# Optimization experiments

Hardware: AMD Instinct MI355X
Metric: run time of the kernel (lower is better)

## Reference

```python
import jax, jax.numpy as jnp
import numpy as np

N_NODES = 50000
N_EDGES = 800000
NUM_REL = 3
NUM_GRAPHS = 512


def _rgcn(x, src, dst, edge_type, Wrel, Wroot, b):
    # PyG RGCNConv with default aggr='mean':
    # out[i] = x[i] @ Wroot + b + sum_r mean_{j in N_r(i)} x[j] @ Wrel[r]
    out = x @ Wroot + b
    for r in range(NUM_REL):
        mask = (edge_type == r)
        h = x @ Wrel[r]                      # transform nodes first (N x d), cheaper than per-edge
        msg = jnp.where(mask[:, None], h[src], jnp.zeros((), x.dtype))  # [E, hid]
        sums = jax.ops.segment_sum(msg, dst, num_segments=N_NODES)
        cnt = jax.ops.segment_sum(mask.astype(x.dtype), dst, num_segments=N_NODES)
        out = out + sums / jnp.maximum(cnt, 1.0)[:, None]
    return out


def setup_inputs() -> dict:
    key = jax.random.key(0)
    ks = jax.random.split(key, 12)
    d, hid, classes = 96, 96, 16
    x = jax.random.normal(ks[0], (N_NODES, d), dtype=jnp.float32)
    edge_index = jax.random.randint(ks[1], (2, N_EDGES), 0, N_NODES, dtype=jnp.int64)
    edge_type = jax.random.randint(ks[2], (N_EDGES,), 0, NUM_REL, dtype=jnp.int64)
    batch = jnp.sort(jax.random.randint(ks[3], (N_NODES,), 0, NUM_GRAPHS, dtype=jnp.int64))
    s1 = 1.0 / np.sqrt(d)
    s2 = 1.0 / np.sqrt(hid)
    return {
        "x": x,
        "edge_index": edge_index,
        "edge_type": edge_type,
        "batch": batch,
        "Wrel1": jax.random.normal(ks[4], (NUM_REL, d, hid), dtype=jnp.float32) * s1,
        "Wroot1": jax.random.normal(ks[5], (d, hid), dtype=jnp.float32) * s1,
        "b1": jnp.zeros((hid,), dtype=jnp.float32),
        "Wrel2": jax.random.normal(ks[6], (NUM_REL, hid, hid), dtype=jnp.float32) * s2,
        "Wroot2": jax.random.normal(ks[7], (hid, hid), dtype=jnp.float32) * s2,
        "b2": jnp.zeros((hid,), dtype=jnp.float32),
        "Wlin": jax.random.normal(ks[8], (hid, classes), dtype=jnp.float32) * s2,
        "blin": jnp.zeros((classes,), dtype=jnp.float32),
    }


def reference(x, edge_index, edge_type, batch, Wrel1, Wroot1, b1, Wrel2, Wroot2, b2, Wlin, blin):
    src, dst = edge_index[0], edge_index[1]
    h = jax.nn.relu(_rgcn(x, src, dst, edge_type, Wrel1, Wroot1, b1))
    h = jax.nn.relu(_rgcn(h, src, dst, edge_type, Wrel2, Wroot2, b2))
    # global mean pool over graphs
    sums = jax.ops.segment_sum(h, batch, num_segments=NUM_GRAPHS)          # [G, hid]
    cnt = jax.ops.segment_sum(jnp.ones((h.shape[0],), h.dtype), batch, num_segments=NUM_GRAPHS)
    pooled = sums / jnp.maximum(cnt, 1.0)[:, None]
    return pooled @ Wlin + blin
```

## Files before the change

kernel.cpp:

```cpp
#include <hip/hip_runtime.h>


#define THREADS 256

typedef __attribute__((ext_vector_type(8))) short short8v;
typedef __attribute__((ext_vector_type(4))) float f32x4;

__device__ __forceinline__ unsigned short f2bf(float f) {
  union { float f; unsigned u; } v; v.f = f;
  unsigned r = v.u + 0x7FFF + ((v.u >> 16) & 1);
  return (unsigned short)(r >> 16);
}
__device__ __forceinline__ float bf2f(unsigned short b) {
  union { unsigned u; float f; } v; v.u = ((unsigned)b) << 16;
  return v.f;
}
__device__ __forceinline__ float bits2f(unsigned u) {
  union { unsigned u; float f; } v; v.u = u;
  return v.f;
}

__global__ __launch_bounds__(256) void k_packW(
    const float* __restrict__ Wrel1, const float* __restrict__ Wroot1,
    const float* __restrict__ Wrel2, const float* __restrict__ Wroot2,
    unsigned short* __restrict__ PBh, unsigned short* __restrict__ PBl)
{
  int lay = blockIdx.x / 144;
  int idx = (blockIdx.x % 144) * 256 + threadIdx.x;
  const float* Wroot = lay ? Wroot2 : Wroot1;
  const float* Wrel  = lay ? Wrel2  : Wrel1;
  int j    = idx & 7;
  int lane = (idx >> 3) & 63;
  int CT   = (idx >> 9) % 24;
  int ks   = (idx >> 9) / 24;
  int k    = ks * 32 + (lane >> 4) * 8 + j;
  int col  = CT * 16 + (lane & 15);
  int m    = col / 96, jj = col % 96;
  float f  = (m == 0) ? Wroot[k * 96 + jj]
                      : Wrel[((size_t)(m - 1) * 96 + k) * 96 + jj];
  unsigned short h = f2bf(f);
  PBh[(size_t)lay * 36864 + idx] = h;
  PBl[(size_t)lay * 36864 + idx] = f2bf(f - bf2f(h));
}

__global__ __launch_bounds__(256) void k_convX(
    const float4* __restrict__ X4, unsigned short* __restrict__ Xh,
    unsigned short* __restrict__ Xl, int n4)
{
  int i = blockIdx.x * THREADS + threadIdx.x;
  if (i >= n4) return;
  float4 v = X4[i];
  ushort4 h, l;
  h.x = f2bf(v.x); l.x = f2bf(v.x - bf2f(h.x));
  h.y = f2bf(v.y); l.y = f2bf(v.y - bf2f(h.y));
  h.z = f2bf(v.z); l.z = f2bf(v.z - bf2f(h.z));
  h.w = f2bf(v.w); l.w = f2bf(v.w - bf2f(h.w));
  *(ushort4*)(Xh + (size_t)i * 4) = h;
  *(ushort4*)(Xl + (size_t)i * 4) = l;
}

__global__ __launch_bounds__(256) void k_hist(
    const int* __restrict__ ei, const int* __restrict__ et,
    int* __restrict__ cnt, int* __restrict__ rank, int* __restrict__ bucket,
    int E, int N)
{
  int e = blockIdx.x * THREADS + threadIdx.x;
  if (e >= E) return;
  int b = et[e] * N + ei[E + e];
  bucket[e] = b;
  rank[e] = atomicAdd(&cnt[b], 1);
}

__global__ __launch_bounds__(256) void k_scan1(int* __restrict__ data, int* __restrict__ blockSums)
{
  __shared__ int sh[256];
  int tid = threadIdx.x;
  size_t base = (size_t)blockIdx.x * 1024 + (size_t)tid * 4;
  int4 v = *(const int4*)(data + base);
  int i0 = v.x, i1 = i0 + v.y, i2 = i1 + v.z, i3 = i2 + v.w;
  int tsum = i3;
  sh[tid] = tsum;
  __syncthreads();
  for (int off = 1; off < 256; off <<= 1) {
    int t = (tid >= off) ? sh[tid - off] : 0;
    __syncthreads();
    sh[tid] += t;
    __syncthreads();
  }
  int excl = sh[tid] - tsum;
  int4 o; o.x = i0 + excl; o.y = i1 + excl; o.z = i2 + excl; o.w = i3 + excl;
  *(int4*)(data + base) = o;
  if (tid == 255) blockSums[blockIdx.x] = sh[255];
}

__global__ __launch_bounds__(256) void k_scan2(const int* __restrict__ blockSums,
                                               int* __restrict__ blockOffs, int nb)
{
  __shared__ int sh[256];
  int tid = threadIdx.x;
  int v = (tid < nb) ? blockSums[tid] : 0;
  sh[tid] = v;
  __syncthreads();
  for (int off = 1; off < 256; off <<= 1) {
    int t = (tid >= off) ? sh[tid - off] : 0;
    __syncthreads();
    sh[tid] += t;
    __syncthreads();
  }
  blockOffs[tid] = sh[tid] - v;
}

__global__ __launch_bounds__(256) void k_scan3(int* __restrict__ data, const int* __restrict__ blockOffs)
{
  int tid = threadIdx.x;
  size_t base = (size_t)blockIdx.x * 1024 + (size_t)tid * 4;
  int add = blockOffs[blockIdx.x];
  int4 v = *(const int4*)(data + base);
  v.x += add; v.y += add; v.z += add; v.w += add;
  *(int4*)(data + base) = v;
}

__global__ __launch_bounds__(256) void k_scatter(
    const int* __restrict__ ei, const int* __restrict__ offs,
    const int* __restrict__ rank, const int* __restrict__ bucket,
    int* __restrict__ payload, int E)
{
  int e = blockIdx.x * THREADS + threadIdx.x;
  if (e >= E) return;
  int b = bucket[e];
  int base = (b == 0) ? 0 : offs[b - 1];
  payload[base + rank[e]] = ei[e];
}

__global__ __launch_bounds__(256) void k_gemm(
    const unsigned short* __restrict__ Xh, const unsigned short* __restrict__ Xl,
    const unsigned short* __restrict__ PBh, const unsigned short* __restrict__ PBl,
    float* __restrict__ Yroot, unsigned short* __restrict__ Hrel, int nRows)
{
  int wv = threadIdx.x >> 6, lane = threadIdx.x & 63;
  int lr = lane & 15, lq = lane >> 4;
  int r0 = blockIdx.x * 64;

  f32x4 acc[4][6];
#pragma unroll
  for (int rt = 0; rt < 4; ++rt)
#pragma unroll
    for (int ct = 0; ct < 6; ++ct) acc[rt][ct] = (f32x4){0.f, 0.f, 0.f, 0.f};

#pragma unroll 1
  for (int ks = 0; ks < 3; ++ks) {
    short8v Ah[4], Al[4];
#pragma unroll
    for (int rt = 0; rt < 4; ++rt) {
      int row = r0 + rt * 16 + lr;
      if (row >= nRows) row = nRows - 1;
      size_t off = (size_t)row * 96 + ks * 32 + lq * 8;
      Ah[rt] = *(const short8v*)(Xh + off);
      Al[rt] = *(const short8v*)(Xl + off);
    }
#pragma unroll
    for (int ct = 0; ct < 6; ++ct) {
      int CT = wv * 6 + ct;
      size_t boff = ((size_t)(ks * 24 + CT) * 64 + lane) * 8;
      short8v Bh = *(const short8v*)(PBh + boff);
      short8v Bl = *(const short8v*)(PBl + boff);
#pragma unroll
      for (int rt = 0; rt < 4; ++rt) {
        acc[rt][ct] = __builtin_amdgcn_mfma_f32_16x16x32_bf16(Ah[rt], Bh, acc[rt][ct], 0, 0, 0);
        acc[rt][ct] = __builtin_amdgcn_mfma_f32_16x16x32_bf16(Al[rt], Bh, acc[rt][ct], 0, 0, 0);
        acc[rt][ct] = __builtin_amdgcn_mfma_f32_16x16x32_bf16(Ah[rt], Bl, acc[rt][ct], 0, 0, 0);
      }
    }
  }

  if (wv == 0) {
#pragma unroll
    for (int rt = 0; rt < 4; ++rt)
#pragma unroll
      for (int q = 0; q < 4; ++q) {
        int row = r0 + rt * 16 + lq * 4 + q;
        if (row < nRows) {
          float* yp = Yroot + (size_t)row * 96 + lr;
#pragma unroll
          for (int ct = 0; ct < 6; ++ct) yp[ct * 16] = acc[rt][ct][q];
        }
      }
  } else {
    int r = wv - 1;
#pragma unroll
    for (int rt = 0; rt < 4; ++rt)
#pragma unroll
      for (int q = 0; q < 4; ++q) {
        int row = r0 + rt * 16 + lq * 4 + q;
        if (row < nRows) {
          unsigned short* hp = Hrel + ((size_t)r * nRows + row) * 96 + lr;
#pragma unroll
          for (int ct = 0; ct < 6; ++ct) hp[ct * 16] = f2bf(acc[rt][ct][q]);
        }
      }
  }
}

__global__ __launch_bounds__(256) void k_agg3(
    const float* __restrict__ Yroot, const unsigned short* __restrict__ Hrel,
    const int* __restrict__ offs, const int* __restrict__ payload,
    const float* __restrict__ bias,
    unsigned int* outH, unsigned int* outL, unsigned int* outF, int N)
{
  int node = blockIdx.x * 16 + (threadIdx.x >> 4);
  int l = threadIdx.x & 15;
  if (node >= N) return;

  const float2* yp = (const float2*)(Yroot + (size_t)node * 96) + 3 * l;
  const float2* bp = (const float2*)bias + 3 * l;
  float2 y0 = yp[0], y1 = yp[1], y2 = yp[2];
  float2 b0 = bp[0], b1 = bp[1], b2 = bp[2];
  float v[6];
  v[0] = y0.x + b0.x; v[1] = y0.y + b0.y;
  v[2] = y1.x + b1.x; v[3] = y1.y + b1.y;
  v[4] = y2.x + b2.x; v[5] = y2.y + b2.y;

#pragma unroll
  for (int r = 0; r < 3; ++r) {
    int bkt = r * N + node;
    int s = (bkt == 0) ? 0 : offs[bkt - 1];
    int e = offs[bkt];
    const unsigned int* base = (const unsigned int*)(Hrel + (size_t)r * N * 96);
    float a[6] = {0.f, 0.f, 0.f, 0.f, 0.f, 0.f};
    int t = s;
    for (; t + 3 < e; t += 4) {
      int p0 = payload[t], p1 = payload[t + 1], p2 = payload[t + 2], p3 = payload[t + 3];
      const unsigned int* h0 = base + (size_t)p0 * 48 + 3 * l;
      const unsigned int* h1 = base + (size_t)p1 * 48 + 3 * l;
      const unsigned int* h2 = base + (size_t)p2 * 48 + 3 * l;
      const unsigned int* h3 = base + (size_t)p3 * 48 + 3 * l;
      unsigned u0 = h0[0], u1 = h0[1], u2 = h0[2];
      unsigned w0 = h1[0], w1 = h1[1], w2 = h1[2];
      unsigned x0 = h2[0], x1 = h2[1], x2 = h2[2];
      unsigned z0 = h3[0], z1 = h3[1], z2 = h3[2];
      a[0] += bits2f(u0 << 16); a[1] += bits2f(u0 & 0xFFFF0000u);
      a[2] += bits2f(u1 << 16); a[3] += bits2f(u1 & 0xFFFF0000u);
      a[4] += bits2f(u2 << 16); a[5] += bits2f(u2 & 0xFFFF0000u);
      a[0] += bits2f(w0 << 16); a[1] += bits2f(w0 & 0xFFFF0000u);
      a[2] += bits2f(w1 << 16); a[3] += bits2f(w1 & 0xFFFF0000u);
      a[4] += bits2f(w2 << 16); a[5] += bits2f(w2 & 0xFFFF0000u);
      a[0] += bits2f(x0 << 16); a[1] += bits2f(x0 & 0xFFFF0000u);
      a[2] += bits2f(x1 << 16); a[3] += bits2f(x1 & 0xFFFF0000u);
      a[4] += bits2f(x2 << 16); a[5] += bits2f(x2 & 0xFFFF0000u);
      a[0] += bits2f(z0 << 16); a[1] += bits2f(z0 & 0xFFFF0000u);
      a[2] += bits2f(z1 << 16); a[3] += bits2f(z1 & 0xFFFF0000u);
      a[4] += bits2f(z2 << 16); a[5] += bits2f(z2 & 0xFFFF0000u);
    }
    for (; t < e; ++t) {
      const unsigned int* h0 = base + (size_t)payload[t] * 48 + 3 * l;
      unsigned u0 = h0[0], u1 = h0[1], u2 = h0[2];
      a[0] += bits2f(u0 << 16); a[1] += bits2f(u0 & 0xFFFF0000u);
      a[2] += bits2f(u1 << 16); a[3] += bits2f(u1 & 0xFFFF0000u);
      a[4] += bits2f(u2 << 16); a[5] += bits2f(u2 & 0xFFFF0000u);
    }
    float inv = (e > s) ? 1.0f / (float)(e - s) : 0.0f;
#pragma unroll
    for (int i = 0; i < 6; ++i) v[i] += a[i] * inv;
  }
#pragma unroll
  for (int i = 0; i < 6; ++i) v[i] = fmaxf(v[i], 0.f);

  size_t ob = (size_t)node * 48 + 3 * l;
  if (outF) {
    outF[ob]     = ((unsigned)f2bf(v[1]) << 16) | f2bf(v[0]);
    outF[ob + 1] = ((unsigned)f2bf(v[3]) << 16) | f2bf(v[2]);
    outF[ob + 2] = ((unsigned)f2bf(v[5]) << 16) | f2bf(v[4]);
  } else {
    unsigned short h[6], lo[6];
#pragma unroll
    for (int i = 0; i < 6; ++i) { h[i] = f2bf(v[i]); lo[i] = f2bf(v[i] - bf2f(h[i])); }
    outH[ob]     = ((unsigned)h[1] << 16) | h[0];
    outH[ob + 1] = ((unsigned)h[3] << 16) | h[2];
    outH[ob + 2] = ((unsigned)h[5] << 16) | h[4];
    outL[ob]     = ((unsigned)lo[1] << 16) | lo[0];
    outL[ob + 1] = ((unsigned)lo[3] << 16) | lo[2];
    outL[ob + 2] = ((unsigned)lo[5] << 16) | lo[4];
  }
}

__global__ __launch_bounds__(256) void k_poolfinal(
    const unsigned int* __restrict__ H, const int* __restrict__ batch,
    const float* __restrict__ Wlin, const float* __restrict__ blin,
    float* __restrict__ out, int N, int G)
{
  int g = blockIdx.x;
  int tid = threadIdx.x;
  int lo = 0, hi = N;
  while (lo < hi) { int m = (lo + hi) >> 1; if (batch[m] < g) lo = m + 1; else hi = m; }
  int s = lo; hi = N;
  while (lo < hi) { int m = (lo + hi) >> 1; if (batch[m] < g + 1) lo = m + 1; else hi = m; }
  int e = lo;

  int grp = tid >> 4, l = tid & 15;
  float a[6] = {0.f, 0.f, 0.f, 0.f, 0.f, 0.f};
  for (int i = s + grp; i < e; i += 16) {
    const unsigned int* hp = H + (size_t)i * 48 + 3 * l;
    unsigned u0 = hp[0], u1 = hp[1], u2 = hp[2];
    a[0] += bits2f(u0 << 16); a[1] += bits2f(u0 & 0xFFFF0000u);
    a[2] += bits2f(u1 << 16); a[3] += bits2f(u1 & 0xFFFF0000u);
    a[4] += bits2f(u2 << 16); a[5] += bits2f(u2 & 0xFFFF0000u);
  }
  __shared__ float sh[16][96];
  __shared__ float pooled[96];
#pragma unroll
  for (int i = 0; i < 6; ++i) sh[grp][6 * l + i] = a[i];
  __syncthreads();
  if (tid < 96) {
    float t = 0.f;
#pragma unroll
    for (int j = 0; j < 16; ++j) t += sh[j][tid];
    float inv = (e > s) ? 1.0f / (float)(e - s) : 0.0f;
    pooled[tid] = t * inv;
  }
  __syncthreads();
  if (tid < 16) {
    float acc = blin[tid];
    for (int k = 0; k < 96; ++k) acc = fmaf(pooled[k], Wlin[k * 16 + tid], acc);
    out[(size_t)g * 16 + tid] = acc;
  }
}

extern "C" void kernel_launch(void* const* d_in, const int* in_sizes, int n_in,
                              void* d_out, int out_size, void* d_ws, size_t ws_size,
                              hipStream_t stream)
{
  const float* x      = (const float*)d_in[0];
  const int*   ei     = (const int*)d_in[1];
  const int*   et     = (const int*)d_in[2];
  const int*   batch  = (const int*)d_in[3];
  const float* Wrel1  = (const float*)d_in[4];
  const float* Wroot1 = (const float*)d_in[5];
  const float* b1     = (const float*)d_in[6];
  const float* Wrel2  = (const float*)d_in[7];
  const float* Wroot2 = (const float*)d_in[8];
  const float* b2     = (const float*)d_in[9];
  const float* Wlin   = (const float*)d_in[10];
  const float* blin   = (const float*)d_in[11];
  float* out = (float*)d_out;
  (void)n_in; (void)ws_size;

  int N = in_sizes[0] / 96;
  int E = in_sizes[1] / 2;
  int G = out_size / 16;
  int NB = 3 * N;
  int nb1 = (NB + 1023) / 1024;
  int SCAN = nb1 * 1024;

  char* w = (char*)d_ws;
  size_t o = 0;
  auto carve = [&](size_t bytes) -> char* {
    char* p = w + o;
    o = (o + bytes + 255) & ~(size_t)255;
    return p;
  };
  float*          Yroot = (float*)carve((size_t)N * 96 * 4);
  unsigned short* Hrel  = (unsigned short*)carve((size_t)3 * N * 96 * 2);
  unsigned short* Xh    = (unsigned short*)carve((size_t)N * 96 * 2);
  unsigned short* Xl    = (unsigned short*)carve((size_t)N * 96 * 2);
  unsigned short* Hout  = (unsigned short*)carve((size_t)N * 96 * 2);
  unsigned short* PBh   = (unsigned short*)carve((size_t)2 * 36864 * 2);
  unsigned short* PBl   = (unsigned short*)carve((size_t)2 * 36864 * 2);
  int*            offs  = (int*)carve((size_t)SCAN * 4);
  int*            blockSums = (int*)carve(256 * 4);
  int*            blockOffs = (int*)carve(256 * 4);
  int*            rank  = (int*)carve((size_t)E * 4);
  int*            bucket= (int*)carve((size_t)E * 4);
  int*            payload = (int*)carve((size_t)E * 4);

  hipMemsetAsync(offs, 0, (size_t)SCAN * 4, stream);

  k_packW<<<288, THREADS, 0, stream>>>(Wrel1, Wroot1, Wrel2, Wroot2, PBh, PBl);
  k_convX<<<(N * 24 + THREADS - 1) / THREADS, THREADS, 0, stream>>>(
      (const float4*)x, Xh, Xl, N * 24);

  k_hist<<<(E + THREADS - 1) / THREADS, THREADS, 0, stream>>>(ei, et, offs, rank, bucket, E, N);
  k_scan1<<<nb1, THREADS, 0, stream>>>(offs, blockSums);
  k_scan2<<<1, THREADS, 0, stream>>>(blockSums, blockOffs, nb1);
  k_scan3<<<nb1, THREADS, 0, stream>>>(offs, blockOffs);
  k_scatter<<<(E + THREADS - 1) / THREADS, THREADS, 0, stream>>>(ei, offs, rank, bucket, payload, E);

  int gg = (N + 63) / 64;
  int ag = (N + 15) / 16;

  k_gemm<<<gg, THREADS, 0, stream>>>(Xh, Xl, PBh, PBl, Yroot, Hrel, N);
  k_agg3<<<ag, THREADS, 0, stream>>>(Yroot, Hrel, offs, payload, b1,
                                     (unsigned int*)Xh, (unsigned int*)Xl, nullptr, N);
  k_gemm<<<gg, THREADS, 0, stream>>>(Xh, Xl, PBh + 36864, PBl + 36864, Yroot, Hrel, N);
  k_agg3<<<ag, THREADS, 0, stream>>>(Yroot, Hrel, offs, payload, b2,
                                     nullptr, nullptr, (unsigned int*)Hout, N);

  k_poolfinal<<<G, THREADS, 0, stream>>>((const unsigned int*)Hout, batch, Wlin, blin, out, N, G);
}
```

Measured before the change: 303.1 us.

## Fuse prep kernels, convert x inside GEMM, shrink payload, vectorize GEMM stores

Merges weight packing and the edge histogram into a single launch, and drops the separate x-to-bf16 split kernel by converting fp32 x to hi/lo bf16 inside the first GEMM. The neighbour index payload is stored as 16-bit values, halving its gather traffic; this relies on node ids fitting in 16 bits, which does not hold for 50000 nodes beyond 65535? (50000 < 65536, so it fits). GEMM epilogue stores are made contiguous per lane by permuting the column layout, with compensating permutations of layer-2 weights, bias indexing and the final Wlin. Together these aim to cut launch overhead and memory traffic, at the cost of permuted intermediate layouts that must stay consistent.

```diff
diff --git a/kernel.cpp b/kernel.cpp
--- a/kernel.cpp
+++ b/kernel.cpp
@@ -19,56 +19,44 @@
   union { unsigned u; float f; } v; v.u = u;
   return v.f;
 }
-
-__global__ __launch_bounds__(256) void k_packW(
+__device__ __forceinline__ unsigned packbf(float a, float b) {
+  return ((unsigned)f2bf(b) << 16) | f2bf(a);
+}
+
+__global__ __launch_bounds__(256) void k_prep(
     const float* __restrict__ Wrel1, const float* __restrict__ Wroot1,
     const float* __restrict__ Wrel2, const float* __restrict__ Wroot2,
-    unsigned short* __restrict__ PBh, unsigned short* __restrict__ PBl)
-{
-  int lay = blockIdx.x / 144;
-  int idx = (blockIdx.x % 144) * 256 + threadIdx.x;
-  const float* Wroot = lay ? Wroot2 : Wroot1;
-  const float* Wrel  = lay ? Wrel2  : Wrel1;
-  int j    = idx & 7;
-  int lane = (idx >> 3) & 63;
-  int CT   = (idx >> 9) % 24;
-  int ks   = (idx >> 9) / 24;
-  int k    = ks * 32 + (lane >> 4) * 8 + j;
-  int col  = CT * 16 + (lane & 15);
-  int m    = col / 96, jj = col % 96;
-  float f  = (m == 0) ? Wroot[k * 96 + jj]
-                      : Wrel[((size_t)(m - 1) * 96 + k) * 96 + jj];
-  unsigned short h = f2bf(f);
-  PBh[(size_t)lay * 36864 + idx] = h;
-  PBl[(size_t)lay * 36864 + idx] = f2bf(f - bf2f(h));
-}
-
-__global__ __launch_bounds__(256) void k_convX(
-    const float4* __restrict__ X4, unsigned short* __restrict__ Xh,
-    unsigned short* __restrict__ Xl, int n4)
-{
-  int i = blockIdx.x * THREADS + threadIdx.x;
-  if (i >= n4) return;
-  float4 v = X4[i];
-  ushort4 h, l;
-  h.x = f2bf(v.x); l.x = f2bf(v.x - bf2f(h.x));
-  h.y = f2bf(v.y); l.y = f2bf(v.y - bf2f(h.y));
-  h.z = f2bf(v.z); l.z = f2bf(v.z - bf2f(h.z));
-  h.w = f2bf(v.w); l.w = f2bf(v.w - bf2f(h.w));
-  *(ushort4*)(Xh + (size_t)i * 4) = h;
-  *(ushort4*)(Xl + (size_t)i * 4) = l;
-}
-
-__global__ __launch_bounds__(256) void k_hist(
+    unsigned short* __restrict__ PBh, unsigned short* __restrict__ PBl,
     const int* __restrict__ ei, const int* __restrict__ et,
     int* __restrict__ cnt, int* __restrict__ rank, int* __restrict__ bucket,
     int E, int N)
 {
-  int e = blockIdx.x * THREADS + threadIdx.x;
-  if (e >= E) return;
-  int b = et[e] * N + ei[E + e];
-  bucket[e] = b;
-  rank[e] = atomicAdd(&cnt[b], 1);
+  int bid = blockIdx.x;
+  if (bid < 288) {
+    int lay = bid / 144;
+    int idx = (bid % 144) * 256 + threadIdx.x;
+    const float* Wroot = lay ? Wroot2 : Wroot1;
+    const float* Wrel  = lay ? Wrel2  : Wrel1;
+    int j    = idx & 7;
+    int lane = (idx >> 3) & 63;
+    int CT   = (idx >> 9) % 24;
+    int ks   = (idx >> 9) / 24;
+    int kpos = ks * 32 + (lane >> 4) * 8 + j;
+    int k    = lay ? ((kpos % 6) * 16 + kpos / 6) : kpos;
+    int col  = CT * 16 + (lane & 15);
+    int m    = col / 96, jj = col % 96;
+    float f  = (m == 0) ? Wroot[k * 96 + jj]
+                        : Wrel[((size_t)(m - 1) * 96 + k) * 96 + jj];
+    unsigned short h = f2bf(f);
+    PBh[(size_t)lay * 36864 + idx] = h;
+    PBl[(size_t)lay * 36864 + idx] = f2bf(f - bf2f(h));
+  } else {
+    int e = (bid - 288) * 256 + threadIdx.x;
+    if (e >= E) return;
+    int b = et[e] * N + ei[E + e];
+    bucket[e] = b;
+    rank[e] = atomicAdd(&cnt[b], 1);
+  }
 }
 
 __global__ __launch_bounds__(256) void k_scan1(int* __restrict__ data, int* __restrict__ blockSums)
@@ -123,17 +111,18 @@
 __global__ __launch_bounds__(256) void k_scatter(
     const int* __restrict__ ei, const int* __restrict__ offs,
     const int* __restrict__ rank, const int* __restrict__ bucket,
-    int* __restrict__ payload, int E)
+    unsigned short* __restrict__ payload, int E)
 {
   int e = blockIdx.x * THREADS + threadIdx.x;
   if (e >= E) return;
   int b = bucket[e];
   int base = (b == 0) ? 0 : offs[b - 1];
-  payload[base + rank[e]] = ei[e];
-}
-
+  payload[base + rank[e]] = (unsigned short)ei[e];
+}
+
+template<bool F32IN>
 __global__ __launch_bounds__(256) void k_gemm(
-    const unsigned short* __restrict__ Xh, const unsigned short* __restrict__ Xl,
+    const void* __restrict__ Xin_, const unsigned short* __restrict__ Xl,
     const unsigned short* __restrict__ PBh, const unsigned short* __restrict__ PBl,
     float* __restrict__ Yroot, unsigned short* __restrict__ Hrel, int nRows)
 {
@@ -155,8 +144,20 @@
       int row = r0 + rt * 16 + lr;
       if (row >= nRows) row = nRows - 1;
       size_t off = (size_t)row * 96 + ks * 32 + lq * 8;
-      Ah[rt] = *(const short8v*)(Xh + off);
-      Al[rt] = *(const short8v*)(Xl + off);
+      if (F32IN) {
+        const float4* xp = (const float4*)((const float*)Xin_ + off);
+        float4 va = xp[0], vb = xp[1];
+        float vv[8] = {va.x, va.y, va.z, va.w, vb.x, vb.y, vb.z, vb.w};
+#pragma unroll
+        for (int j = 0; j < 8; ++j) {
+          unsigned short h = f2bf(vv[j]);
+          Ah[rt][j] = (short)h;
+          Al[rt][j] = (short)f2bf(vv[j] - bf2f(h));
+        }
+      } else {
+        Ah[rt] = *(const short8v*)((const unsigned short*)Xin_ + off);
+        Al[rt] = *(const short8v*)(Xl + off);
+      }
     }
 #pragma unroll
     for (int ct = 0; ct < 6; ++ct) {
@@ -180,9 +181,10 @@
       for (int q = 0; q < 4; ++q) {
         int row = r0 + rt * 16 + lq * 4 + q;
         if (row < nRows) {
-          float* yp = Yroot + (size_t)row * 96 + lr;
-#pragma unroll
-          for (int ct = 0; ct < 6; ++ct) yp[ct * 16] = acc[rt][ct][q];
+          float2* yp = (float2*)(Yroot + (size_t)row * 96 + lr * 6);
+          yp[0] = make_float2(acc[rt][0][q], acc[rt][1][q]);
+          yp[1] = make_float2(acc[rt][2][q], acc[rt][3][q]);
+          yp[2] = make_float2(acc[rt][4][q], acc[rt][5][q]);
         }
       }
   } else {
@@ -193,9 +195,10 @@
       for (int q = 0; q < 4; ++q) {
         int row = r0 + rt * 16 + lq * 4 + q;
         if (row < nRows) {
-          unsigned short* hp = Hrel + ((size_t)r * nRows + row) * 96 + lr;
-#pragma unroll
-          for (int ct = 0; ct < 6; ++ct) hp[ct * 16] = f2bf(acc[rt][ct][q]);
+          unsigned* hp = (unsigned*)(Hrel + ((size_t)r * nRows + row) * 96 + lr * 6);
+          hp[0] = packbf(acc[rt][0][q], acc[rt][1][q]);
+          hp[1] = packbf(acc[rt][2][q], acc[rt][3][q]);
+          hp[2] = packbf(acc[rt][4][q], acc[rt][5][q]);
         }
       }
   }
@@ -203,7 +206,7 @@
 
 __global__ __launch_bounds__(256) void k_agg3(
     const float* __restrict__ Yroot, const unsigned short* __restrict__ Hrel,
-    const int* __restrict__ offs, const int* __restrict__ payload,
+    const int* __restrict__ offs, const unsigned short* __restrict__ payload,
     const float* __restrict__ bias,
     unsigned int* outH, unsigned int* outL, unsigned int* outF, int N)
 {
@@ -212,13 +215,11 @@
   if (node >= N) return;
 
   const float2* yp = (const float2*)(Yroot + (size_t)node * 96) + 3 * l;
-  const float2* bp = (const float2*)bias + 3 * l;
   float2 y0 = yp[0], y1 = yp[1], y2 = yp[2];
-  float2 b0 = bp[0], b1 = bp[1], b2 = bp[2];
   float v[6];
-  v[0] = y0.x + b0.x; v[1] = y0.y + b0.y;
-  v[2] = y1.x + b1.x; v[3] = y1.y + b1.y;
-  v[4] = y2.x + b2.x; v[5] = y2.y + b2.y;
+  v[0] = y0.x + bias[l];       v[1] = y0.y + bias[16 + l];
+  v[2] = y1.x + bias[32 + l];  v[3] = y1.y + bias[48 + l];
+  v[4] = y2.x + bias[64 + l];  v[5] = y2.y + bias[80 + l];
 
 #pragma unroll
   for (int r = 0; r < 3; ++r) {
@@ -267,9 +268,9 @@
 
   size_t ob = (size_t)node * 48 + 3 * l;
   if (outF) {
-    outF[ob]     = ((unsigned)f2bf(v[1]) << 16) | f2bf(v[0]);
-    outF[ob + 1] = ((unsigned)f2bf(v[3]) << 16) | f2bf(v[2]);
-    outF[ob + 2] = ((unsigned)f2bf(v[5]) << 16) | f2bf(v[4]);
+    outF[ob]     = packbf(v[0], v[1]);
+    outF[ob + 1] = packbf(v[2], v[3]);
+    outF[ob + 2] = packbf(v[4], v[5]);
   } else {
     unsigned short h[6], lo[6];
 #pragma unroll
@@ -320,7 +321,9 @@
   __syncthreads();
   if (tid < 16) {
     float acc = blin[tid];
-    for (int k = 0; k < 96; ++k) acc = fmaf(pooled[k], Wlin[k * 16 + tid], acc);
+#pragma unroll
+    for (int k = 0; k < 96; ++k)
+      acc = fmaf(pooled[k], Wlin[((k % 6) * 16 + k / 6) * 16 + tid], acc);
     out[(size_t)g * 16 + tid] = acc;
   }
 }
@@ -370,27 +373,25 @@
   int*            blockOffs = (int*)carve(256 * 4);
   int*            rank  = (int*)carve((size_t)E * 4);
   int*            bucket= (int*)carve((size_t)E * 4);
-  int*            payload = (int*)carve((size_t)E * 4);
+  unsigned short* payload = (unsigned short*)carve((size_t)E * 2);
 
   hipMemsetAsync(offs, 0, (size_t)SCAN * 4, stream);
 
-  k_packW<<<288, THREADS, 0, stream>>>(Wrel1, Wroot1, Wrel2, Wroot2, PBh, PBl);
-  k_convX<<<(N * 24 + THREADS - 1) / THREADS, THREADS, 0, stream>>>(
-      (const float4*)x, Xh, Xl, N * 24);
-
-  k_hist<<<(E + THREADS - 1) / THREADS, THREADS, 0, stream>>>(ei, et, offs, rank, bucket, E, N);
+  int histBlocks = (E + THREADS - 1) / THREADS;
+  k_prep<<<288 + histBlocks, THREADS, 0, stream>>>(
+      Wrel1, Wroot1, Wrel2, Wroot2, PBh, PBl, ei, et, offs, rank, bucket, E, N);
   k_scan1<<<nb1, THREADS, 0, stream>>>(offs, blockSums);
   k_scan2<<<1, THREADS, 0, stream>>>(blockSums, blockOffs, nb1);
   k_scan3<<<nb1, THREADS, 0, stream>>>(offs, blockOffs);
-  k_scatter<<<(E + THREADS - 1) / THREADS, THREADS, 0, stream>>>(ei, offs, rank, bucket, payload, E);
+  k_scatter<<<histBlocks, THREADS, 0, stream>>>(ei, offs, rank, bucket, payload, E);
 
   int gg = (N + 63) / 64;
   int ag = (N + 15) / 16;
 
-  k_gemm<<<gg, THREADS, 0, stream>>>(Xh, Xl, PBh, PBl, Yroot, Hrel, N);
+  k_gemm<true><<<gg, THREADS, 0, stream>>>(x, nullptr, PBh, PBl, Yroot, Hrel, N);
   k_agg3<<<ag, THREADS, 0, stream>>>(Yroot, Hrel, offs, payload, b1,
                                      (unsigned int*)Xh, (unsigned int*)Xl, nullptr, N);
-  k_gemm<<<gg, THREADS, 0, stream>>>(Xh, Xl, PBh + 36864, PBl + 36864, Yroot, Hrel, N);
+  k_gemm<false><<<gg, THREADS, 0, stream>>>(Xh, Xl, PBh + 36864, PBl + 36864, Yroot, Hrel, N);
   k_agg3<<<ag, THREADS, 0, stream>>>(Yroot, Hrel, offs, payload, b2,
                                      nullptr, nullptr, (unsigned int*)Hout, N);
 
```

After: 292.1 us. 3.6% less time.
